# Performance work log

Hardware: AMD Instinct MI355X
Metric: run time of the kernel (lower is better)

Reference implementation:

```python
import jax, jax.numpy as jnp
import numpy as np

B, S, E, H, V, OOV = 128, 400, 512, 512, 50257, 50
VEXT = V + OOV


def setup_inputs() -> dict:
    key = jax.random.key(0)
    ks = jax.random.split(key, 20)
    w = lambda k, shp: (0.02 * jax.random.normal(k, shp)).astype(jnp.float32)
    return {
        'input_emb': jax.random.normal(ks[0], (B, 1, E), jnp.float32),
        'input_feed': jax.random.normal(ks[1], (B, 1, H), jnp.float32),
        'hidden': jax.random.normal(ks[2], (1, B, H), jnp.float32),
        'context': jax.random.normal(ks[3], (1, B, H), jnp.float32),
        'states': jax.random.normal(ks[4], (B, S, H), jnp.float32),
        'states_features': jax.random.normal(ks[5], (B, S, H), jnp.float32),
        'source_mask': jnp.ones((B, S), jnp.float32),
        'coverage': jnp.zeros((B, S), jnp.float32),
        'source_ids': jax.random.randint(ks[6], (B, S), 0, VEXT, jnp.int32),
        'W_ic': w(ks[7], (E, H + E)), 'b_ic': jnp.zeros((E,), jnp.float32),
        'W_ih': w(ks[8], (4 * H, E)), 'W_hh': w(ks[9], (4 * H, H)),
        'b_ih': jnp.zeros((4 * H,), jnp.float32), 'b_hh': jnp.zeros((4 * H,), jnp.float32),
        'W_dec': w(ks[10], (H, H)), 'b_att': jnp.zeros((H,), jnp.float32),
        'v_att': w(ks[11], (H,)), 'w_c': w(ks[12], (1,)),
        'W_out': w(ks[13], (H, 2 * H)), 'b_out': jnp.zeros((H,), jnp.float32),
        'W_pg': w(ks[14], (1, H)), 'b_pg': jnp.zeros((1,), jnp.float32),
        'W_v': w(ks[15], (V, H)), 'b_v': jnp.zeros((V,), jnp.float32),
    }


def reference(input_emb, input_feed, hidden, context, states, states_features,
              source_mask, coverage, source_ids,
              W_ic, b_ic, W_ih, W_hh, b_ih, b_hh,
              W_dec, b_att, v_att, w_c, W_out, b_out,
              W_pg, b_pg, W_v, b_v):
    # x = input_context(cat(input_emb, input_feed))  -> [B,1,E]
    x = jnp.concatenate([input_emb, input_feed], axis=2) @ W_ic.T + b_ic
    # single LSTM step (PyTorch gate order i,f,g,o)
    h0, c0 = hidden[0], context[0]                      # [B,H]
    gates = x[:, 0] @ W_ih.T + b_ih + h0 @ W_hh.T + b_hh
    i, f, g, o = jnp.split(gates, 4, axis=-1)
    i, f, o = jax.nn.sigmoid(i), jax.nn.sigmoid(f), jax.nn.sigmoid(o)
    c1 = f * c0 + i * jnp.tanh(g)
    h1 = o * jnp.tanh(c1)                               # rnn_output [B,H]
    # coverage attention
    dec_fea = h1 @ W_dec.T + b_att                      # [B,H]
    e = jnp.tanh(states_features + dec_fea[:, None, :] + w_c * coverage[..., None]) @ v_att  # [B,S]
    e = jnp.where(source_mask > 0, e, jnp.float32(-1e9))
    attn = jax.nn.softmax(e, axis=-1) * source_mask
    attn = attn / (attn.sum(-1, keepdims=True) + 1e-12)  # [B,S]
    ctx = jnp.einsum('bs,bsh->bh', attn, states)
    dec_out = jnp.concatenate([h1, ctx], axis=-1) @ W_out.T + b_out  # decoder_output [B,H]
    coverage_new = coverage + attn
    # pointer-generator mixing
    p_gen = jax.nn.sigmoid(dec_out @ W_pg.T + b_pg)     # [B,1]
    vocab_dist = p_gen * jax.nn.softmax(dec_out @ W_v.T + b_v, axis=-1)  # [B,V]
    ext = jnp.zeros((B, VEXT), vocab_dist.dtype).at[:, :V].set(vocab_dist)
    attn_dist = (1.0 - p_gen) * attn                    # [B,S]
    final = ext.at[jnp.arange(B)[:, None], source_ids].add(attn_dist)  # scatter_add over vocab
    final_dist = final[:, None, :]                      # [B,1,VEXT]
    return (final_dist, p_gen, attn, coverage_new, h1[None], c1[None], dec_out[:, None, :])
```

## Files before the change

kernel.cpp:

```cpp
#include <hip/hip_runtime.h>
#include <hip/hip_bf16.h>

#define B_   128
#define S_   400
#define H_   512
#define V_   50257
#define VX_  50307
#define NBN_ 1571

#define OFF_FINAL 0
#define OFF_PGEN  6439296
#define OFF_ATTN  6439424
#define OFF_COV   6490624
#define OFF_H1    6541824
#define OFF_C1    6607360
#define OFF_DEC   6672896

typedef __attribute__((ext_vector_type(8))) short bf16x8;
typedef __attribute__((ext_vector_type(4))) float f32x4;

static __device__ __forceinline__ float sigmoid_f(float x) {
    return 1.0f / (1.0f + __expf(-x));
}
static __device__ __forceinline__ float tanh_f(float x) {
    return 1.0f - 2.0f / (__expf(2.0f * x) + 1.0f);
}
static __device__ __forceinline__ unsigned int pk2(float x, float y) {
    union { __hip_bfloat162 h; unsigned int u; } cv;
    cv.h = __float22bfloat162_rn(make_float2(x, y));
    return cv.u;
}

__global__ __launch_bounds__(256) void zero_ws(
    float4* __restrict__ fin4, float4* __restrict__ ws4,
    float4* __restrict__ dec4, float4* __restrict__ ctx4,
    float4* __restrict__ pga4)
{
    const int i = blockIdx.x * 256 + threadIdx.x;
    const float4 z = make_float4(0.f, 0.f, 0.f, 0.f);
    if (i < 1609824) fin4[i] = z;
    if (i < 98304)   ws4[i] = z;
    if (i < 16384)   dec4[i] = z;
    if (i < 16384)   ctx4[i] = z;
    if (i < 32)      pga4[i] = z;
}

template <int NT>
__global__ __launch_bounds__(256) void gemm_mfma(
    const float* __restrict__ A1, const float* __restrict__ W1, int ldw1, int kwo1,
    const float* __restrict__ A2, const float* __restrict__ W2, int ldw2, int kwo2,
    const float* __restrict__ bias1,
    float* __restrict__ C, int N,
    const float* __restrict__ wpg, float* __restrict__ pgen_acc)
{
    __shared__ __align__(16) unsigned short As[128 * 40];
    __shared__ __align__(16) unsigned short Ws[NT * 16 * 40];
    const int tid  = threadIdx.x;
    const int bn0  = blockIdx.x * (NT * 16);
    const int lane = tid & 63;
    const int wv   = tid >> 6;
    const int quad = lane >> 4;
    const int col  = lane & 15;

    f32x4 acc[2][NT];
#pragma unroll
    for (int i = 0; i < 2; ++i)
#pragma unroll
        for (int j = 0; j < NT; ++j) acc[i][j] = (f32x4){0.f, 0.f, 0.f, 0.f};

    const int ar = tid >> 1;
    const int ac = (tid & 1) << 4;
    const int wr = (NT == 8) ? (tid >> 1) : (tid >> 2);
    const int wc = (NT == 8) ? ((tid & 1) << 4) : ((tid & 3) << 3);
    const int wrg = (bn0 + wr < N) ? (bn0 + wr) : (N - 1);

    const int Ktot = (A2 != nullptr) ? 1024 : 512;
    const int KC   = Ktot / gridDim.y;
    const int kg0  = blockIdx.y * KC;
    const int nsteps = KC >> 5;

    const float* ApB[2];
    const float* WpB[2];
    ApB[0] = A1 + (long)ar * 512 + ac;
    WpB[0] = W1 + (long)wrg * ldw1 + kwo1 + wc;
    ApB[1] = A2 ? (A2 + (long)ar * 512 + ac) : ApB[0];
    WpB[1] = W2 ? (W2 + (long)wrg * ldw2 + kwo2 + wc) : WpB[0];

    float4 aC[4], wC[NT / 2], aN[4], wN[NT / 2];

    auto fetch = [&](int s, float4* a, float4* w) {
        const int kg = kg0 + (s << 5);
        const int ph = kg >> 9;
        const int k0 = kg & 511;
        const float* Ap = ApB[ph] + k0;
        const float* Wp = WpB[ph] + k0;
#pragma unroll
        for (int i = 0; i < 4; ++i) a[i] = *(const float4*)(Ap + i * 4);
#pragma unroll
        for (int i = 0; i < NT / 2; ++i) w[i] = *(const float4*)(Wp + i * 4);
    };

    fetch(0, aC, wC);
    for (int s = 0; s < nsteps; ++s) {
        __syncthreads();
        uint4* apd = (uint4*)&As[ar * 40 + ac];
        apd[0] = make_uint4(pk2(aC[0].x, aC[0].y), pk2(aC[0].z, aC[0].w),
                            pk2(aC[1].x, aC[1].y), pk2(aC[1].z, aC[1].w));
        apd[1] = make_uint4(pk2(aC[2].x, aC[2].y), pk2(aC[2].z, aC[2].w),
                            pk2(aC[3].x, aC[3].y), pk2(aC[3].z, aC[3].w));
        uint4* wpd = (uint4*)&Ws[wr * 40 + wc];
        wpd[0] = make_uint4(pk2(wC[0].x, wC[0].y), pk2(wC[0].z, wC[0].w),
                            pk2(wC[1].x, wC[1].y), pk2(wC[1].z, wC[1].w));
        if (NT == 8)
            wpd[1] = make_uint4(pk2(wC[2].x, wC[2].y), pk2(wC[2].z, wC[2].w),
                                pk2(wC[3].x, wC[3].y), pk2(wC[3].z, wC[3].w));
        __syncthreads();

        if (s + 1 < nsteps) fetch(s + 1, aN, wN);

        const bf16x8 aF0 = *(const bf16x8*)&As[(wv * 32 + col) * 40 + quad * 8];
        const bf16x8 aF1 = *(const bf16x8*)&As[(wv * 32 + 16 + col) * 40 + quad * 8];
#pragma unroll
        for (int ni = 0; ni < NT; ++ni) {
            const bf16x8 bF = *(const bf16x8*)&Ws[(ni * 16 + col) * 40 + quad * 8];
            acc[0][ni] = __builtin_amdgcn_mfma_f32_16x16x32_bf16(aF0, bF, acc[0][ni], 0, 0, 0);
            acc[1][ni] = __builtin_amdgcn_mfma_f32_16x16x32_bf16(aF1, bF, acc[1][ni], 0, 0, 0);
        }
#pragma unroll
        for (int i = 0; i < 4; ++i) aC[i] = aN[i];
#pragma unroll
        for (int i = 0; i < NT / 2; ++i) wC[i] = wN[i];
    }

    const bool split = (gridDim.y > 1);
    const bool addb  = (!split) || (blockIdx.y == 0);

    float pgp[2][4];
#pragma unroll
    for (int i = 0; i < 2; ++i)
#pragma unroll
        for (int r = 0; r < 4; ++r) pgp[i][r] = 0.f;

#pragma unroll
    for (int mi = 0; mi < 2; ++mi) {
#pragma unroll
        for (int ni = 0; ni < NT; ++ni) {
            const int n = bn0 + ni * 16 + col;
            if (n < N) {
                const float bv = addb ? bias1[n] : 0.f;
                const float wpv = wpg ? wpg[n] : 0.f;
#pragma unroll
                for (int r = 0; r < 4; ++r) {
                    const int m = wv * 32 + mi * 16 + quad * 4 + r;
                    const float v = acc[mi][ni][r] + bv;
                    if (split) atomicAdd(&C[(long)m * N + n], v);
                    else       C[(long)m * N + n] = v;
                    pgp[mi][r] += v * wpv;
                }
            }
        }
    }
    if (wpg) {
#pragma unroll
        for (int mi = 0; mi < 2; ++mi)
#pragma unroll
            for (int r = 0; r < 4; ++r) {
                float v = pgp[mi][r];
                v += __shfl_xor(v, 1); v += __shfl_xor(v, 2);
                v += __shfl_xor(v, 4); v += __shfl_xor(v, 8);
                if (col == 0) {
                    const int m = wv * 32 + mi * 16 + quad * 4 + r;
                    atomicAdd(&pgen_acc[m], v);
                }
            }
    }
}

__global__ __launch_bounds__(256) void pack_a(
    const float* __restrict__ A, unsigned short* __restrict__ Apk)
{
    const int u  = blockIdx.x * 256 + threadIdx.x;
    const int c  = u & 15;
    const int q  = (u >> 4) & 3;
    const int mt = (u >> 6) & 7;
    const int sl = u >> 9;
    const float* src = A + (long)(mt * 16 + c) * 512 + sl * 32 + q * 8;
    const float4 x = *(const float4*)src;
    const float4 y = *(const float4*)(src + 4);
    *(uint4*)(Apk + (long)u * 8) = make_uint4(pk2(x.x, x.y), pk2(x.z, x.w),
                                              pk2(y.x, y.y), pk2(y.z, y.w));
}

__global__ __launch_bounds__(256, 5) void vocab_gemm(
    const unsigned short* __restrict__ Apk, const float* __restrict__ W,
    const float* __restrict__ bias, float* __restrict__ C, int N,
    float* __restrict__ ps, int nbn)
{
    __shared__ __align__(16) unsigned short Ws[32 * 512];
    const int tid  = threadIdx.x;
    const int lane = tid & 63;
    const int w    = tid >> 6;
    const int quad = lane >> 4;
    const int c    = lane & 15;
    const int nb   = blockIdx.x;

#pragma unroll
    for (int i = 0; i < 8; ++i) {
        const int r  = i * 4 + w;
        const int rg = (nb * 32 + r < N) ? (nb * 32 + r) : (N - 1);
        const float* src = W + (long)rg * 512 + (lane << 3);
        const float4 x = *(const float4*)src;
        const float4 y = *(const float4*)(src + 4);
        const int a16 = (r << 6) + (lane ^ (r & 7));
        *(uint4*)&Ws[a16 << 3] = make_uint4(pk2(x.x, x.y), pk2(x.z, x.w),
                                            pk2(y.x, y.y), pk2(y.z, y.w));
    }

    f32x4 acc[2][2];
#pragma unroll
    for (int mi = 0; mi < 2; ++mi)
#pragma unroll
        for (int nj = 0; nj < 2; ++nj) acc[mi][nj] = (f32x4){0.f, 0.f, 0.f, 0.f};

    bf16x8 aP0[2], aP1[2], aP2[2], aP3[2];
    auto loadA = [&](int sl, bf16x8* dst) {
#pragma unroll
        for (int mi = 0; mi < 2; ++mi) {
            const int u = ((sl * 8 + (w * 2 + mi)) * 4 + quad) * 16 + c;
            dst[mi] = *(const bf16x8*)(Apk + (long)u * 8);
        }
    };
    loadA(0, aP0); loadA(1, aP1); loadA(2, aP2); loadA(3, aP3);
    __syncthreads();

#pragma unroll
    for (int sl = 0; sl < 16; ++sl) {
        bf16x8* cur = ((sl & 3) == 0) ? aP0 : ((sl & 3) == 1) ? aP1
                    : ((sl & 3) == 2) ? aP2 : aP3;
        const int uk = ((sl << 2) + quad) ^ (c & 7);
        const bf16x8 bF0 = *(const bf16x8*)&Ws[((c << 6) + uk) << 3];
        const bf16x8 bF1 = *(const bf16x8*)&Ws[((((16 + c)) << 6) + uk) << 3];
        acc[0][0] = __builtin_amdgcn_mfma_f32_16x16x32_bf16(cur[0], bF0, acc[0][0], 0, 0, 0);
        acc[0][1] = __builtin_amdgcn_mfma_f32_16x16x32_bf16(cur[0], bF1, acc[0][1], 0, 0, 0);
        acc[1][0] = __builtin_amdgcn_mfma_f32_16x16x32_bf16(cur[1], bF0, acc[1][0], 0, 0, 0);
        acc[1][1] = __builtin_amdgcn_mfma_f32_16x16x32_bf16(cur[1], bF1, acc[1][1], 0, 0, 0);
        if (sl + 4 < 16) loadA(sl + 4, cur);
    }

    const int n0 = nb * 32 + c;
    const int n1 = nb * 32 + 16 + c;
    const bool ok0 = (n0 < N), ok1 = (n1 < N);
    const float bv0 = bias[ok0 ? n0 : (N - 1)];
    const float bv1 = bias[ok1 ? n1 : (N - 1)];
#pragma unroll
    for (int mi = 0; mi < 2; ++mi) {
#pragma unroll
        for (int r = 0; r < 4; ++r) {
            const int m = w * 32 + mi * 16 + quad * 4 + r;
            const float v0 = acc[mi][0][r] + bv0;
            const float v1 = acc[mi][1][r] + bv1;
            if (ok0) C[(long)m * N + n0] = v0;
            if (ok1) C[(long)m * N + n1] = v1;
            float sv = (ok0 ? __expf(v0) : 0.f) + (ok1 ? __expf(v1) : 0.f);
            sv += __shfl_xor(sv, 1); sv += __shfl_xor(sv, 2);
            sv += __shfl_xor(sv, 4); sv += __shfl_xor(sv, 8);
            if (c == 0) ps[(long)m * nbn + nb] = sv;
        }
    }
}

__global__ __launch_bounds__(256) void merge_scatter(
    const float* __restrict__ ps, int nblk,
    const float* __restrict__ pgen_acc, const float* __restrict__ bpg,
    const int* __restrict__ ids, const float* __restrict__ attn,
    float* __restrict__ Srow, float* __restrict__ o_pgen,
    float* __restrict__ final)
{
    __shared__ float sred[4];
    __shared__ float sPG;
    const int b = blockIdx.x, tid = threadIdx.x;
    const float* psb = ps + (long)b * nblk;

    float s = 0.f;
    for (int i = tid; i < nblk; i += 256) s += psb[i];
#pragma unroll
    for (int off = 32; off > 0; off >>= 1) s += __shfl_down(s, off);
    if ((tid & 63) == 0) sred[tid >> 6] = s;
    __syncthreads();
    if (tid == 0) {
        Srow[b] = sred[0] + sred[1] + sred[2] + sred[3];
        const float pg = sigmoid_f(pgen_acc[b] + bpg[0]);
        o_pgen[b] = pg;
        sPG = pg;
    }
    __syncthreads();
    const float omp = 1.0f - sPG;
    for (int sidx = tid; sidx < 400; sidx += 256) {
        const float v = omp * attn[b * 400 + sidx];
        atomicAdd(final + (long)b * VX_ + ids[b * 400 + sidx], v);
    }
}

__global__ __launch_bounds__(256) void lstm_cell(
    const float* __restrict__ gates, const float* __restrict__ bhh,
    const float* __restrict__ c0,
    float* __restrict__ h1, float* __restrict__ c1)
{
    const int idx = blockIdx.x * 256 + threadIdx.x;
    const int m = idx >> 9;
    const int h = idx & 511;
    const float* g = gates + (long)m * 2048;
    const float iv = sigmoid_f(g[h]        + bhh[h]);
    const float fv = sigmoid_f(g[512 + h]  + bhh[512 + h]);
    const float gv = tanh_f   (g[1024 + h] + bhh[1024 + h]);
    const float ov = sigmoid_f(g[1536 + h] + bhh[1536 + h]);
    const float c = fv * c0[idx] + iv * gv;
    c1[idx] = c;
    h1[idx] = ov * tanh_f(c);
}

__global__ __launch_bounds__(256) void attn_scores(
    const float* __restrict__ sfeat, const float* __restrict__ decfea,
    const float* __restrict__ cov, const float* __restrict__ wc,
    const float* __restrict__ vatt, float* __restrict__ e)
{
    const int lane = threadIdx.x & 63;
    const int pair = blockIdx.x * 4 + (threadIdx.x >> 6);
    const int b = pair / 400;
    const float cc = wc[0] * cov[pair];
    const float* sp = sfeat + ((long)pair << 9) + (lane << 3);
    const float* dp = decfea + (b << 9) + (lane << 3);
    const float* vp = vatt + (lane << 3);
    const float4 s0 = *(const float4*)sp, s1 = *(const float4*)(sp + 4);
    const float4 d0 = *(const float4*)dp, d1 = *(const float4*)(dp + 4);
    const float4 v0 = *(const float4*)vp, v1 = *(const float4*)(vp + 4);
    float acc = tanh_f(s0.x + d0.x + cc) * v0.x
              + tanh_f(s0.y + d0.y + cc) * v0.y
              + tanh_f(s0.z + d0.z + cc) * v0.z
              + tanh_f(s0.w + d0.w + cc) * v0.w
              + tanh_f(s1.x + d1.x + cc) * v1.x
              + tanh_f(s1.y + d1.y + cc) * v1.y
              + tanh_f(s1.z + d1.z + cc) * v1.z
              + tanh_f(s1.w + d1.w + cc) * v1.w;
#pragma unroll
    for (int off = 32; off > 0; off >>= 1) acc += __shfl_down(acc, off);
    if (lane == 0) e[pair] = acc;
}

__global__ __launch_bounds__(256) void softmax_ctx(
    const float* __restrict__ e, const float* __restrict__ mask,
    const float* __restrict__ cov, const float* __restrict__ states,
    float* __restrict__ attn, float* __restrict__ covnew,
    float* __restrict__ ctx)
{
    __shared__ float sm[4], sps[4], spms[4];
    __shared__ float s_attn[100];
    const int bx = blockIdx.x;
    const int b = bx >> 2, chunk = bx & 3;
    const int tid = threadIdx.x;

    float vals[2], msk[2];
    float m = -3.0e38f;
#pragma unroll
    for (int it = 0; it < 2; ++it) {
        const int s = tid + (it << 8);
        float mk = 0.f, v = -3.0e38f;
        if (s < 400) {
            mk = mask[b * 400 + s];
            v = (mk > 0.f) ? e[b * 400 + s] : -1.0e9f;
        }
        vals[it] = v; msk[it] = mk;
        m = fmaxf(m, v);
    }
#pragma unroll
    for (int off = 32; off > 0; off >>= 1) m = fmaxf(m, __shfl_down(m, off));
    if ((tid & 63) == 0) sm[tid >> 6] = m;
    __syncthreads();
    const float M = fmaxf(fmaxf(sm[0], sm[1]), fmaxf(sm[2], sm[3]));

    float sp = 0.f, spm = 0.f;
#pragma unroll
    for (int it = 0; it < 2; ++it) {
        const int s = tid + (it << 8);
        float pv = 0.f;
        if (s < 400) pv = __expf(vals[it] - M);
        sp += pv; spm += pv * msk[it];
    }
#pragma unroll
    for (int off = 32; off > 0; off >>= 1) {
        sp += __shfl_down(sp, off);
        spm += __shfl_down(spm, off);
    }
    if ((tid & 63) == 0) { sps[tid >> 6] = sp; spms[tid >> 6] = spm; }
    __syncthreads();
    const float SP = sps[0] + sps[1] + sps[2] + sps[3];
    const float SPM = spms[0] + spms[1] + spms[2] + spms[3];
    const float inv = 1.0f / (SPM + 1e-12f * SP);

    if (tid < 100) {
        const int s = chunk * 100 + tid;
        const float mk = mask[b * 400 + s];
        const float pv = (mk > 0.f) ? __expf(e[b * 400 + s] - M) : 0.f;
        const float a = pv * mk * inv;
        attn[b * 400 + s] = a;
        covnew[b * 400 + s] = cov[b * 400 + s] + a;
        s_attn[tid] = a;
    }
    __syncthreads();

    const int c = tid & 127;
    const int sh = tid >> 7;
    const float* base = states + (long)b * 400 * 512 + (long)chunk * 100 * 512;
    float4 acc = make_float4(0.f, 0.f, 0.f, 0.f);
    for (int i = 0; i < 50; ++i) {
        const int sl = sh + (i << 1);
        const float a = s_attn[sl];
        const float4 st = *(const float4*)(base + (long)sl * 512 + (c << 2));
        acc.x = fmaf(a, st.x, acc.x);
        acc.y = fmaf(a, st.y, acc.y);
        acc.z = fmaf(a, st.z, acc.z);
        acc.w = fmaf(a, st.w, acc.w);
    }
    float* cp = ctx + (b << 9) + (c << 2);
    atomicAdd(cp + 0, acc.x);
    atomicAdd(cp + 1, acc.y);
    atomicAdd(cp + 2, acc.z);
    atomicAdd(cp + 3, acc.w);
}

__global__ __launch_bounds__(256) void final_write(
    const float* __restrict__ logits, const float* __restrict__ Srow,
    const float* __restrict__ o_pgen, float* __restrict__ final)
{
    const int b = blockIdx.y;
    const int tid = threadIdx.x;
    const float sc = o_pgen[b] / Srow[b];
    const int v0 = (blockIdx.x * 256 + tid) << 2;
    if (v0 >= VX_) return;
    const float* row = logits + (long)b * V_;
    float* out = final + (long)b * VX_ + v0;
#pragma unroll
    for (int j = 0; j < 4; ++j) {
        const int v = v0 + j;
        if (v < V_) out[j] += __expf(row[v]) * sc;
    }
}

extern "C" void kernel_launch(void* const* d_in, const int* in_sizes, int n_in,
                              void* d_out, int out_size, void* d_ws, size_t ws_size,
                              hipStream_t stream)
{
    const float* input_emb  = (const float*)d_in[0];
    const float* input_feed = (const float*)d_in[1];
    const float* hidden     = (const float*)d_in[2];
    const float* context    = (const float*)d_in[3];
    const float* states     = (const float*)d_in[4];
    const float* sfeat      = (const float*)d_in[5];
    const float* mask       = (const float*)d_in[6];
    const float* cov        = (const float*)d_in[7];
    const int*   src_ids    = (const int*)d_in[8];
    const float* W_ic  = (const float*)d_in[9];
    const float* b_ic  = (const float*)d_in[10];
    const float* W_ih  = (const float*)d_in[11];
    const float* W_hh  = (const float*)d_in[12];
    const float* b_ih  = (const float*)d_in[13];
    const float* b_hh  = (const float*)d_in[14];
    const float* W_dec = (const float*)d_in[15];
    const float* b_att = (const float*)d_in[16];
    const float* v_att = (const float*)d_in[17];
    const float* w_c   = (const float*)d_in[18];
    const float* W_out = (const float*)d_in[19];
    const float* b_out = (const float*)d_in[20];
    const float* W_pg  = (const float*)d_in[21];
    const float* b_pg  = (const float*)d_in[22];
    const float* W_v   = (const float*)d_in[23];
    const float* b_v   = (const float*)d_in[24];

    float* out = (float*)d_out;
    float* o_final = out + OFF_FINAL;
    float* o_pgen  = out + OFF_PGEN;
    float* o_attn  = out + OFF_ATTN;
    float* o_cov   = out + OFF_COV;
    float* o_h1    = out + OFF_H1;
    float* o_c1    = out + OFF_C1;
    float* o_dec   = out + OFF_DEC;

    float* ws = (float*)d_ws;
    float* w_x      = ws;
    float* w_decfea = ws + 65536;
    float* w_gates  = ws + 131072;
    float* w_ps     = ws;
    float* w_e      = ws + 393344;
    float* w_ctx    = ws + 444544;
    float* w_logits = ws + 510080;
    unsigned short* w_apk = (unsigned short*)(ws + 6942976);
    float* w_Srow   = ws + 6975744;
    float* w_pga    = ws + 6976000;

    const dim3 blk(256);
    zero_ws<<<6290, blk, 0, stream>>>((float4*)o_final, (float4*)ws,
                                      (float4*)o_dec, (float4*)w_ctx,
                                      (float4*)w_pga);
    gemm_mfma<4><<<dim3(8, 8), blk, 0, stream>>>(
        input_emb, W_ic, 1024, 0, input_feed, W_ic, 1024, 512,
        b_ic, w_x, 512, nullptr, nullptr);
    gemm_mfma<4><<<dim3(32, 4), blk, 0, stream>>>(
        w_x, W_ih, 512, 0, hidden, W_hh, 512, 0,
        b_ih, w_gates, 2048, nullptr, nullptr);
    lstm_cell<<<256, blk, 0, stream>>>(w_gates, b_hh, context, o_h1, o_c1);
    gemm_mfma<4><<<dim3(8, 4), blk, 0, stream>>>(
        o_h1, W_dec, 512, 0, nullptr, nullptr, 0, 0,
        b_att, w_decfea, 512, nullptr, nullptr);
    attn_scores<<<12800, blk, 0, stream>>>(sfeat, w_decfea, cov, w_c, v_att, w_e);
    softmax_ctx<<<512, blk, 0, stream>>>(w_e, mask, cov, states,
                                         o_attn, o_cov, w_ctx);
    gemm_mfma<4><<<dim3(8, 8), blk, 0, stream>>>(
        o_h1, W_out, 1024, 0, w_ctx, W_out, 1024, 512,
        b_out, o_dec, 512, W_pg, w_pga);
    pack_a<<<32, blk, 0, stream>>>(o_dec, w_apk);
    vocab_gemm<<<NBN_, blk, 0, stream>>>(
        w_apk, W_v, b_v, w_logits, V_, w_ps, NBN_);
    merge_scatter<<<128, blk, 0, stream>>>(w_ps, NBN_, w_pga, b_pg,
                                           src_ids, o_attn,
                                           w_Srow, o_pgen, o_final);
    final_write<<<dim3(50, 128), blk, 0, stream>>>(w_logits, w_Srow,
                                                   o_pgen, o_final);
}
```

Measured before the change: 453.8 us.

## Store bf16 exp-logits, drop final zeroing, write final directly then scatter

The vocab GEMM now stages exp(logit) values in LDS and writes them as bf16 into a padded buffer with vectorised stores, instead of writing fp32 logits. final_write overwrites the output, including zeroing the OOV tail, rather than reading and adding, so the large memset of the final distribution is removed. The pointer scatter-add moves into a separate kernel that runs after final_write. This cuts several large passes over the 128x50k output and halves the logit traffic, at the cost of bf16 rounding on the probabilities and one extra launch.

```diff
diff --git a/kernel.cpp b/kernel.cpp
--- a/kernel.cpp
+++ b/kernel.cpp
@@ -7,6 +7,7 @@
 #define V_   50257
 #define VX_  50307
 #define NBN_ 1571
+#define ELD_ 50264
 
 #define OFF_FINAL 0
 #define OFF_PGEN  6439296
@@ -30,19 +31,22 @@
     cv.h = __float22bfloat162_rn(make_float2(x, y));
     return cv.u;
 }
+static __device__ __forceinline__ unsigned short bf16_1(float x) {
+    union { __hip_bfloat16 h; unsigned short u; } cv;
+    cv.h = __float2bfloat16(x);
+    return cv.u;
+}
 
 __global__ __launch_bounds__(256) void zero_ws(
-    float4* __restrict__ fin4, float4* __restrict__ ws4,
-    float4* __restrict__ dec4, float4* __restrict__ ctx4,
-    float4* __restrict__ pga4)
+    float4* __restrict__ ws4, float4* __restrict__ dec4,
+    float4* __restrict__ ctx4, float4* __restrict__ pga4)
 {
     const int i = blockIdx.x * 256 + threadIdx.x;
     const float4 z = make_float4(0.f, 0.f, 0.f, 0.f);
-    if (i < 1609824) fin4[i] = z;
-    if (i < 98304)   ws4[i] = z;
-    if (i < 16384)   dec4[i] = z;
-    if (i < 16384)   ctx4[i] = z;
-    if (i < 32)      pga4[i] = z;
+    if (i < 98304) ws4[i] = z;
+    if (i < 16384) dec4[i] = z;
+    if (i < 16384) ctx4[i] = z;
+    if (i < 32)    pga4[i] = z;
 }
 
 template <int NT>
@@ -193,7 +197,7 @@
 
 __global__ __launch_bounds__(256, 5) void vocab_gemm(
     const unsigned short* __restrict__ Apk, const float* __restrict__ W,
-    const float* __restrict__ bias, float* __restrict__ C, int N,
+    const float* __restrict__ bias, unsigned short* __restrict__ E,
     float* __restrict__ ps, int nbn)
 {
     __shared__ __align__(16) unsigned short Ws[32 * 512];
@@ -203,6 +207,7 @@
     const int quad = lane >> 4;
     const int c    = lane & 15;
     const int nb   = blockIdx.x;
+    const int N    = V_;
 
 #pragma unroll
     for (int i = 0; i < 8; ++i) {
@@ -247,6 +252,8 @@
         if (sl + 4 < 16) loadA(sl + 4, cur);
     }
 
+    __syncthreads();
+    unsigned short* elds = Ws;
     const int n0 = nb * 32 + c;
     const int n1 = nb * 32 + 16 + c;
     const bool ok0 = (n0 < N), ok1 = (n1 < N);
@@ -257,30 +264,52 @@
 #pragma unroll
         for (int r = 0; r < 4; ++r) {
             const int m = w * 32 + mi * 16 + quad * 4 + r;
-            const float v0 = acc[mi][0][r] + bv0;
-            const float v1 = acc[mi][1][r] + bv1;
-            if (ok0) C[(long)m * N + n0] = v0;
-            if (ok1) C[(long)m * N + n1] = v1;
-            float sv = (ok0 ? __expf(v0) : 0.f) + (ok1 ? __expf(v1) : 0.f);
+            const float ev0 = ok0 ? __expf(acc[mi][0][r] + bv0) : 0.f;
+            const float ev1 = ok1 ? __expf(acc[mi][1][r] + bv1) : 0.f;
+            elds[m * 34 + c]      = bf16_1(ev0);
+            elds[m * 34 + 16 + c] = bf16_1(ev1);
+            float sv = ev0 + ev1;
             sv += __shfl_xor(sv, 1); sv += __shfl_xor(sv, 2);
             sv += __shfl_xor(sv, 4); sv += __shfl_xor(sv, 8);
             if (c == 0) ps[(long)m * nbn + nb] = sv;
         }
     }
-}
-
-__global__ __launch_bounds__(256) void merge_scatter(
+    __syncthreads();
+    {
+        const int r = tid >> 1;
+        const int h = tid & 1;
+        const int ncol = nb * 32 + h * 16;
+        const unsigned short* src = &elds[r * 34 + h * 16];
+        if (ncol + 16 <= ELD_) {
+            uint4 v;
+            v.x = src[0] | ((unsigned)src[1] << 16);
+            v.y = src[2] | ((unsigned)src[3] << 16);
+            v.z = src[4] | ((unsigned)src[5] << 16);
+            v.w = src[6] | ((unsigned)src[7] << 16);
+            uint4 v2;
+            v2.x = src[8]  | ((unsigned)src[9] << 16);
+            v2.y = src[10] | ((unsigned)src[11] << 16);
+            v2.z = src[12] | ((unsigned)src[13] << 16);
+            v2.w = src[14] | ((unsigned)src[15] << 16);
+            *(uint4*)&E[(long)r * ELD_ + ncol] = v;
+            *(uint4*)&E[(long)r * ELD_ + ncol + 8] = v2;
+        } else {
+            for (int j = 0; j < 16; ++j) {
+                const int n = ncol + j;
+                if (n < N) E[(long)r * ELD_ + n] = src[j];
+            }
+        }
+    }
+}
+
+__global__ __launch_bounds__(256) void row_merge(
     const float* __restrict__ ps, int nblk,
     const float* __restrict__ pgen_acc, const float* __restrict__ bpg,
-    const int* __restrict__ ids, const float* __restrict__ attn,
-    float* __restrict__ Srow, float* __restrict__ o_pgen,
-    float* __restrict__ final)
+    float* __restrict__ Srow, float* __restrict__ o_pgen)
 {
     __shared__ float sred[4];
-    __shared__ float sPG;
     const int b = blockIdx.x, tid = threadIdx.x;
     const float* psb = ps + (long)b * nblk;
-
     float s = 0.f;
     for (int i = tid; i < nblk; i += 256) s += psb[i];
 #pragma unroll
@@ -289,15 +318,7 @@
     __syncthreads();
     if (tid == 0) {
         Srow[b] = sred[0] + sred[1] + sred[2] + sred[3];
-        const float pg = sigmoid_f(pgen_acc[b] + bpg[0]);
-        o_pgen[b] = pg;
-        sPG = pg;
-    }
-    __syncthreads();
-    const float omp = 1.0f - sPG;
-    for (int sidx = tid; sidx < 400; sidx += 256) {
-        const float v = omp * attn[b * 400 + sidx];
-        atomicAdd(final + (long)b * VX_ + ids[b * 400 + sidx], v);
+        o_pgen[b] = sigmoid_f(pgen_acc[b] + bpg[0]);
     }
 }
 
@@ -429,7 +450,7 @@
 }
 
 __global__ __launch_bounds__(256) void final_write(
-    const float* __restrict__ logits, const float* __restrict__ Srow,
+    const unsigned short* __restrict__ E, const float* __restrict__ Srow,
     const float* __restrict__ o_pgen, float* __restrict__ final)
 {
     const int b = blockIdx.y;
@@ -437,12 +458,37 @@
     const float sc = o_pgen[b] / Srow[b];
     const int v0 = (blockIdx.x * 256 + tid) << 2;
     if (v0 >= VX_) return;
-    const float* row = logits + (long)b * V_;
+    const unsigned short* row = E + (long)b * ELD_;
     float* out = final + (long)b * VX_ + v0;
-#pragma unroll
-    for (int j = 0; j < 4; ++j) {
-        const int v = v0 + j;
-        if (v < V_) out[j] += __expf(row[v]) * sc;
+    if (v0 + 4 <= V_) {
+        const uint2 u = *(const uint2*)&row[v0];
+        float4 o;
+        o.x = __bfloat162float(*(const __hip_bfloat16*)&((const unsigned short*)&u)[0]) * sc;
+        o.y = __bfloat162float(*(const __hip_bfloat16*)&((const unsigned short*)&u)[1]) * sc;
+        o.z = __bfloat162float(*(const __hip_bfloat16*)&((const unsigned short*)&u)[2]) * sc;
+        o.w = __bfloat162float(*(const __hip_bfloat16*)&((const unsigned short*)&u)[3]) * sc;
+        *(float4*)out = o;
+    } else {
+#pragma unroll
+        for (int j = 0; j < 4; ++j) {
+            const int v = v0 + j;
+            if (v < VX_)
+                out[j] = (v < V_)
+                    ? __bfloat162float(*(const __hip_bfloat16*)&row[v]) * sc
+                    : 0.f;
+        }
+    }
+}
+
+__global__ __launch_bounds__(256) void scatter_kernel(
+    const int* __restrict__ ids, const float* __restrict__ attn,
+    const float* __restrict__ pgen, float* __restrict__ final)
+{
+    const int s = blockIdx.x * 256 + threadIdx.x;
+    const int b = blockIdx.y;
+    if (s < 400) {
+        const float v = (1.0f - pgen[b]) * attn[b * 400 + s];
+        atomicAdd(final + (long)b * VX_ + ids[b * 400 + s], v);
     }
 }
 
@@ -492,15 +538,14 @@
     float* w_ps     = ws;
     float* w_e      = ws + 393344;
     float* w_ctx    = ws + 444544;
-    float* w_logits = ws + 510080;
-    unsigned short* w_apk = (unsigned short*)(ws + 6942976);
+    unsigned short* w_elog = (unsigned short*)(ws + 510080);
+    unsigned short* w_apk  = (unsigned short*)(ws + 6942976);
     float* w_Srow   = ws + 6975744;
     float* w_pga    = ws + 6976000;
 
     const dim3 blk(256);
-    zero_ws<<<6290, blk, 0, stream>>>((float4*)o_final, (float4*)ws,
-                                      (float4*)o_dec, (float4*)w_ctx,
-                                      (float4*)w_pga);
+    zero_ws<<<385, blk, 0, stream>>>((float4*)ws, (float4*)o_dec,
+                                     (float4*)w_ctx, (float4*)w_pga);
     gemm_mfma<4><<<dim3(8, 8), blk, 0, stream>>>(
         input_emb, W_ic, 1024, 0, input_feed, W_ic, 1024, 512,
         b_ic, w_x, 512, nullptr, nullptr);
@@ -519,10 +564,9 @@
         b_out, o_dec, 512, W_pg, w_pga);
     pack_a<<<32, blk, 0, stream>>>(o_dec, w_apk);
     vocab_gemm<<<NBN_, blk, 0, stream>>>(
-        w_apk, W_v, b_v, w_logits, V_, w_ps, NBN_);
-    merge_scatter<<<128, blk, 0, stream>>>(w_ps, NBN_, w_pga, b_pg,
-                                           src_ids, o_attn,
-                                           w_Srow, o_pgen, o_final);
-    final_write<<<dim3(50, 128), blk, 0, stream>>>(w_logits, w_Srow,
+        w_apk, W_v, b_v, w_elog, w_ps, NBN_);
+    row_merge<<<128, blk, 0, stream>>>(w_ps, NBN_, w_pga, b_pg, w_Srow, o_pgen);
+    final_write<<<dim3(50, 128), blk, 0, stream>>>(w_elog, w_Srow,
                                                    o_pgen, o_final);
-}
+    scatter_kernel<<<dim3(2, 128), blk, 0, stream>>>(src_ids, o_attn, o_pgen, o_final);
+}
```

After: 432.2 us. 4.8% less time.

## Fuse vocab GEMM, softmax normalization and final write via grid barrier

Applied to the files above, without the earlier changes.

The vocab GEMM becomes a persistent kernel with 786 blocks, each handling up to two 32-column panels. Partial exp-sums are reduced across the grid with a software global barrier, per-row scales are computed, and the normalized probabilities are written straight from registers into the final output. This removes the logits round-trip through global memory, the full zeroing of the final buffer, and the separate merge and final_write launches. In exchange it depends on all 786 blocks being co-resident (occupancy 4 per CU) to avoid deadlock, uses two accumulator sets that raise register pressure, and moves the scatter-add into a small kernel that runs afterward.

```diff
diff --git a/kernel.cpp b/kernel.cpp
--- a/kernel.cpp
+++ b/kernel.cpp
@@ -7,6 +7,7 @@
 #define V_   50257
 #define VX_  50307
 #define NBN_ 1571
+#define GRIDV_ 786
 
 #define OFF_FINAL 0
 #define OFF_PGEN  6439296
@@ -31,18 +32,35 @@
     return cv.u;
 }
 
+static __device__ __forceinline__ void gbar(unsigned int* ctr, unsigned int target) {
+    __syncthreads();
+    if (threadIdx.x == 0) {
+        __threadfence();
+        __hip_atomic_fetch_add(ctr, 1u, __ATOMIC_ACQ_REL, __HIP_MEMORY_SCOPE_AGENT);
+        while (__hip_atomic_load(ctr, __ATOMIC_ACQUIRE, __HIP_MEMORY_SCOPE_AGENT) < target)
+            __builtin_amdgcn_s_sleep(4);
+        __threadfence();
+    }
+    __syncthreads();
+}
+
 __global__ __launch_bounds__(256) void zero_ws(
-    float4* __restrict__ fin4, float4* __restrict__ ws4,
-    float4* __restrict__ dec4, float4* __restrict__ ctx4,
-    float4* __restrict__ pga4)
+    float4* __restrict__ ws4, float4* __restrict__ dec4,
+    float4* __restrict__ ctx4, float4* __restrict__ pga4,
+    float* __restrict__ fin, unsigned int* __restrict__ ctr)
 {
     const int i = blockIdx.x * 256 + threadIdx.x;
     const float4 z = make_float4(0.f, 0.f, 0.f, 0.f);
-    if (i < 1609824) fin4[i] = z;
-    if (i < 98304)   ws4[i] = z;
-    if (i < 16384)   dec4[i] = z;
-    if (i < 16384)   ctx4[i] = z;
-    if (i < 32)      pga4[i] = z;
+    if (i < 98304) ws4[i] = z;
+    if (i < 16384) dec4[i] = z;
+    if (i < 16384) ctx4[i] = z;
+    if (i < 32)    pga4[i] = z;
+    if (i == 0)    *ctr = 0u;
+    if (i < 128 * (VX_ - V_)) {
+        const int b = i / 50;
+        const int v = V_ + (i - b * 50);
+        fin[(long)b * VX_ + v] = 0.f;
+    }
 }
 
 template <int NT>
@@ -191,38 +209,26 @@
                                               pk2(y.x, y.y), pk2(y.z, y.w));
 }
 
-__global__ __launch_bounds__(256, 5) void vocab_gemm(
+__global__ __launch_bounds__(256, 4) void vocab_fused(
     const unsigned short* __restrict__ Apk, const float* __restrict__ W,
-    const float* __restrict__ bias, float* __restrict__ C, int N,
-    float* __restrict__ ps, int nbn)
+    const float* __restrict__ bias, float* __restrict__ ps,
+    const float* __restrict__ pgen_acc, const float* __restrict__ bpg,
+    float* __restrict__ scale, float* __restrict__ o_pgen,
+    float* __restrict__ final, unsigned int* __restrict__ ctr)
 {
     __shared__ __align__(16) unsigned short Ws[32 * 512];
+    __shared__ float sred[4];
     const int tid  = threadIdx.x;
     const int lane = tid & 63;
     const int w    = tid >> 6;
     const int quad = lane >> 4;
     const int c    = lane & 15;
-    const int nb   = blockIdx.x;
-
-#pragma unroll
-    for (int i = 0; i < 8; ++i) {
-        const int r  = i * 4 + w;
-        const int rg = (nb * 32 + r < N) ? (nb * 32 + r) : (N - 1);
-        const float* src = W + (long)rg * 512 + (lane << 3);
-        const float4 x = *(const float4*)src;
-        const float4 y = *(const float4*)(src + 4);
-        const int a16 = (r << 6) + (lane ^ (r & 7));
-        *(uint4*)&Ws[a16 << 3] = make_uint4(pk2(x.x, x.y), pk2(x.z, x.w),
-                                            pk2(y.x, y.y), pk2(y.z, y.w));
-    }
-
-    f32x4 acc[2][2];
-#pragma unroll
-    for (int mi = 0; mi < 2; ++mi)
-#pragma unroll
-        for (int nj = 0; nj < 2; ++nj) acc[mi][nj] = (f32x4){0.f, 0.f, 0.f, 0.f};
-
-    bf16x8 aP0[2], aP1[2], aP2[2], aP3[2];
+    const int bid  = blockIdx.x;
+    const int p0 = bid;
+    const int p1 = bid + GRIDV_;
+
+    f32x4 accA[2][2], accB[2][2];
+
     auto loadA = [&](int sl, bf16x8* dst) {
 #pragma unroll
         for (int mi = 0; mi < 2; ++mi) {
@@ -230,75 +236,106 @@
             dst[mi] = *(const bf16x8*)(Apk + (long)u * 8);
         }
     };
-    loadA(0, aP0); loadA(1, aP1); loadA(2, aP2); loadA(3, aP3);
-    __syncthreads();
-
-#pragma unroll
-    for (int sl = 0; sl < 16; ++sl) {
-        bf16x8* cur = ((sl & 3) == 0) ? aP0 : ((sl & 3) == 1) ? aP1
-                    : ((sl & 3) == 2) ? aP2 : aP3;
-        const int uk = ((sl << 2) + quad) ^ (c & 7);
-        const bf16x8 bF0 = *(const bf16x8*)&Ws[((c << 6) + uk) << 3];
-        const bf16x8 bF1 = *(const bf16x8*)&Ws[((((16 + c)) << 6) + uk) << 3];
-        acc[0][0] = __builtin_amdgcn_mfma_f32_16x16x32_bf16(cur[0], bF0, acc[0][0], 0, 0, 0);
-        acc[0][1] = __builtin_amdgcn_mfma_f32_16x16x32_bf16(cur[0], bF1, acc[0][1], 0, 0, 0);
-        acc[1][0] = __builtin_amdgcn_mfma_f32_16x16x32_bf16(cur[1], bF0, acc[1][0], 0, 0, 0);
-        acc[1][1] = __builtin_amdgcn_mfma_f32_16x16x32_bf16(cur[1], bF1, acc[1][1], 0, 0, 0);
-        if (sl + 4 < 16) loadA(sl + 4, cur);
-    }
-
-    const int n0 = nb * 32 + c;
-    const int n1 = nb * 32 + 16 + c;
-    const bool ok0 = (n0 < N), ok1 = (n1 < N);
-    const float bv0 = bias[ok0 ? n0 : (N - 1)];
-    const float bv1 = bias[ok1 ? n1 : (N - 1)];
-#pragma unroll
-    for (int mi = 0; mi < 2; ++mi) {
-#pragma unroll
-        for (int r = 0; r < 4; ++r) {
-            const int m = w * 32 + mi * 16 + quad * 4 + r;
-            const float v0 = acc[mi][0][r] + bv0;
-            const float v1 = acc[mi][1][r] + bv1;
-            if (ok0) C[(long)m * N + n0] = v0;
-            if (ok1) C[(long)m * N + n1] = v1;
-            float sv = (ok0 ? __expf(v0) : 0.f) + (ok1 ? __expf(v1) : 0.f);
-            sv += __shfl_xor(sv, 1); sv += __shfl_xor(sv, 2);
-            sv += __shfl_xor(sv, 4); sv += __shfl_xor(sv, 8);
-            if (c == 0) ps[(long)m * nbn + nb] = sv;
-        }
-    }
-}
-
-__global__ __launch_bounds__(256) void merge_scatter(
-    const float* __restrict__ ps, int nblk,
-    const float* __restrict__ pgen_acc, const float* __restrict__ bpg,
-    const int* __restrict__ ids, const float* __restrict__ attn,
-    float* __restrict__ Srow, float* __restrict__ o_pgen,
-    float* __restrict__ final)
-{
-    __shared__ float sred[4];
-    __shared__ float sPG;
-    const int b = blockIdx.x, tid = threadIdx.x;
-    const float* psb = ps + (long)b * nblk;
-
-    float s = 0.f;
-    for (int i = tid; i < nblk; i += 256) s += psb[i];
-#pragma unroll
-    for (int off = 32; off > 0; off >>= 1) s += __shfl_down(s, off);
-    if ((tid & 63) == 0) sred[tid >> 6] = s;
-    __syncthreads();
-    if (tid == 0) {
-        Srow[b] = sred[0] + sred[1] + sred[2] + sred[3];
-        const float pg = sigmoid_f(pgen_acc[b] + bpg[0]);
-        o_pgen[b] = pg;
-        sPG = pg;
-    }
-    __syncthreads();
-    const float omp = 1.0f - sPG;
-    for (int sidx = tid; sidx < 400; sidx += 256) {
-        const float v = omp * attn[b * 400 + sidx];
-        atomicAdd(final + (long)b * VX_ + ids[b * 400 + sidx], v);
-    }
+
+    auto do_panel = [&](int nb, f32x4 (&acc)[2][2]) {
+#pragma unroll
+        for (int mi = 0; mi < 2; ++mi)
+#pragma unroll
+            for (int nj = 0; nj < 2; ++nj) acc[mi][nj] = (f32x4){0.f, 0.f, 0.f, 0.f};
+#pragma unroll
+        for (int i = 0; i < 8; ++i) {
+            const int r  = i * 4 + w;
+            const int rg = (nb * 32 + r < V_) ? (nb * 32 + r) : (V_ - 1);
+            const float* src = W + (long)rg * 512 + (lane << 3);
+            const float4 x = *(const float4*)src;
+            const float4 y = *(const float4*)(src + 4);
+            const int a16 = (r << 6) + (lane ^ (r & 7));
+            *(uint4*)&Ws[a16 << 3] = make_uint4(pk2(x.x, x.y), pk2(x.z, x.w),
+                                                pk2(y.x, y.y), pk2(y.z, y.w));
+        }
+        bf16x8 aP0[2], aP1[2], aP2[2], aP3[2];
+        loadA(0, aP0); loadA(1, aP1); loadA(2, aP2); loadA(3, aP3);
+        __syncthreads();
+#pragma unroll
+        for (int sl = 0; sl < 16; ++sl) {
+            bf16x8* cur = ((sl & 3) == 0) ? aP0 : ((sl & 3) == 1) ? aP1
+                        : ((sl & 3) == 2) ? aP2 : aP3;
+            const int uk = ((sl << 2) + quad) ^ (c & 7);
+            const bf16x8 bF0 = *(const bf16x8*)&Ws[((c << 6) + uk) << 3];
+            const bf16x8 bF1 = *(const bf16x8*)&Ws[(((16 + c) << 6) + uk) << 3];
+            acc[0][0] = __builtin_amdgcn_mfma_f32_16x16x32_bf16(cur[0], bF0, acc[0][0], 0, 0, 0);
+            acc[0][1] = __builtin_amdgcn_mfma_f32_16x16x32_bf16(cur[0], bF1, acc[0][1], 0, 0, 0);
+            acc[1][0] = __builtin_amdgcn_mfma_f32_16x16x32_bf16(cur[1], bF0, acc[1][0], 0, 0, 0);
+            acc[1][1] = __builtin_amdgcn_mfma_f32_16x16x32_bf16(cur[1], bF1, acc[1][1], 0, 0, 0);
+            if (sl + 4 < 16) loadA(sl + 4, cur);
+        }
+        const int n0 = nb * 32 + c;
+        const int n1 = nb * 32 + 16 + c;
+        const bool ok0 = (n0 < V_), ok1 = (n1 < V_);
+        const float bv0 = bias[ok0 ? n0 : (V_ - 1)];
+        const float bv1 = bias[ok1 ? n1 : (V_ - 1)];
+#pragma unroll
+        for (int mi = 0; mi < 2; ++mi) {
+#pragma unroll
+            for (int r = 0; r < 4; ++r) {
+                const int m = w * 32 + mi * 16 + quad * 4 + r;
+                float sv = (ok0 ? __expf(acc[mi][0][r] + bv0) : 0.f)
+                         + (ok1 ? __expf(acc[mi][1][r] + bv1) : 0.f);
+                sv += __shfl_xor(sv, 1); sv += __shfl_xor(sv, 2);
+                sv += __shfl_xor(sv, 4); sv += __shfl_xor(sv, 8);
+                if (c == 0)
+                    __hip_atomic_store(&ps[(long)m * NBN_ + nb], sv,
+                                       __ATOMIC_RELAXED, __HIP_MEMORY_SCOPE_AGENT);
+            }
+        }
+        __syncthreads();
+    };
+
+    do_panel(p0, accA);
+    if (p1 < NBN_) do_panel(p1, accB);
+
+    gbar(ctr, GRIDV_);
+
+    if (bid < 128) {
+        const float* psb = ps + (long)bid * NBN_;
+        float s = 0.f;
+        for (int i = tid; i < NBN_; i += 256)
+            s += __hip_atomic_load(&psb[i], __ATOMIC_RELAXED, __HIP_MEMORY_SCOPE_AGENT);
+#pragma unroll
+        for (int off = 32; off > 0; off >>= 1) s += __shfl_down(s, off);
+        if ((tid & 63) == 0) sred[tid >> 6] = s;
+        __syncthreads();
+        if (tid == 0) {
+            const float S = sred[0] + sred[1] + sred[2] + sred[3];
+            const float pg = sigmoid_f(pgen_acc[bid] + bpg[0]);
+            o_pgen[bid] = pg;
+            __hip_atomic_store(&scale[bid], pg / S,
+                               __ATOMIC_RELAXED, __HIP_MEMORY_SCOPE_AGENT);
+        }
+    }
+
+    gbar(ctr, 2u * GRIDV_);
+
+    auto writeout = [&](int nb, f32x4 (&acc)[2][2]) {
+        const int n0 = nb * 32 + c;
+        const int n1 = nb * 32 + 16 + c;
+        const bool ok0 = (n0 < V_), ok1 = (n1 < V_);
+        const float bv0 = bias[ok0 ? n0 : (V_ - 1)];
+        const float bv1 = bias[ok1 ? n1 : (V_ - 1)];
+#pragma unroll
+        for (int mi = 0; mi < 2; ++mi) {
+#pragma unroll
+            for (int r = 0; r < 4; ++r) {
+                const int m = w * 32 + mi * 16 + quad * 4 + r;
+                const float sc = __hip_atomic_load(&scale[m], __ATOMIC_RELAXED,
+                                                   __HIP_MEMORY_SCOPE_AGENT);
+                if (ok0) final[(long)m * VX_ + n0] = __expf(acc[mi][0][r] + bv0) * sc;
+                if (ok1) final[(long)m * VX_ + n1] = __expf(acc[mi][1][r] + bv1) * sc;
+            }
+        }
+    };
+    writeout(p0, accA);
+    if (p1 < NBN_) writeout(p1, accB);
 }
 
 __global__ __launch_bounds__(256) void lstm_cell(
@@ -428,21 +465,15 @@
     atomicAdd(cp + 3, acc.w);
 }
 
-__global__ __launch_bounds__(256) void final_write(
-    const float* __restrict__ logits, const float* __restrict__ Srow,
-    const float* __restrict__ o_pgen, float* __restrict__ final)
-{
+__global__ __launch_bounds__(256) void scatter_kernel(
+    const int* __restrict__ ids, const float* __restrict__ attn,
+    const float* __restrict__ pgen, float* __restrict__ final)
+{
+    const int s = blockIdx.x * 256 + threadIdx.x;
     const int b = blockIdx.y;
-    const int tid = threadIdx.x;
-    const float sc = o_pgen[b] / Srow[b];
-    const int v0 = (blockIdx.x * 256 + tid) << 2;
-    if (v0 >= VX_) return;
-    const float* row = logits + (long)b * V_;
-    float* out = final + (long)b * VX_ + v0;
-#pragma unroll
-    for (int j = 0; j < 4; ++j) {
-        const int v = v0 + j;
-        if (v < V_) out[j] += __expf(row[v]) * sc;
+    if (s < 400) {
+        const float v = (1.0f - pgen[b]) * attn[b * 400 + s];
+        atomicAdd(final + (long)b * VX_ + ids[b * 400 + s], v);
     }
 }
 
@@ -492,15 +523,15 @@
     float* w_ps     = ws;
     float* w_e      = ws + 393344;
     float* w_ctx    = ws + 444544;
-    float* w_logits = ws + 510080;
-    unsigned short* w_apk = (unsigned short*)(ws + 6942976);
-    float* w_Srow   = ws + 6975744;
+    unsigned short* w_apk  = (unsigned short*)(ws + 6942976);
+    float* w_scale  = ws + 6975744;
     float* w_pga    = ws + 6976000;
+    unsigned int* w_ctr = (unsigned int*)(ws + 6976128);
 
     const dim3 blk(256);
-    zero_ws<<<6290, blk, 0, stream>>>((float4*)o_final, (float4*)ws,
-                                      (float4*)o_dec, (float4*)w_ctx,
-                                      (float4*)w_pga);
+    zero_ws<<<385, blk, 0, stream>>>((float4*)ws, (float4*)o_dec,
+                                     (float4*)w_ctx, (float4*)w_pga,
+                                     o_final, w_ctr);
     gemm_mfma<4><<<dim3(8, 8), blk, 0, stream>>>(
         input_emb, W_ic, 1024, 0, input_feed, W_ic, 1024, 512,
         b_ic, w_x, 512, nullptr, nullptr);
@@ -518,11 +549,7 @@
         o_h1, W_out, 1024, 0, w_ctx, W_out, 1024, 512,
         b_out, o_dec, 512, W_pg, w_pga);
     pack_a<<<32, blk, 0, stream>>>(o_dec, w_apk);
-    vocab_gemm<<<NBN_, blk, 0, stream>>>(
-        w_apk, W_v, b_v, w_logits, V_, w_ps, NBN_);
-    merge_scatter<<<128, blk, 0, stream>>>(w_ps, NBN_, w_pga, b_pg,
-                                           src_ids, o_attn,
-                                           w_Srow, o_pgen, o_final);
-    final_write<<<dim3(50, 128), blk, 0, stream>>>(w_logits, w_Srow,
-                                                   o_pgen, o_final);
-}
+    vocab_fused<<<GRIDV_, blk, 0, stream>>>(
+        w_apk, W_v, b_v, w_ps, w_pga, b_pg, w_scale, o_pgen, o_final, w_ctr);
+    scatter_kernel<<<dim3(2, 128), blk, 0, stream>>>(src_ids, o_attn, o_pgen, o_final);
+}
```

Result: slower. 710.9 us (+56.6%).
